# Kernel optimization log

Measured on AMD Instinct MI355X. Metric: run time of the kernel, lower is better.

The kernel has to match this reference:

```python
import jax, jax.numpy as jnp
import numpy as np

N, E, H = 50000, 800000, 4
DIM_IN, DIM_H, DIM_OUT, EDGE_DIM = 128, 64, 64, 16
NEG_ATT, NEG_OUT, BN_EPS = 0.2, 0.1, 1e-5


def batch_norm(x, gamma, beta):
    # training-mode BatchNorm1d over the node dimension
    mu = x.mean(0)
    var = x.var(0)
    return (x - mu) * jax.lax.rsqrt(var + BN_EPS) * gamma + beta


def gat_conv(x, src, dst, eattr, W, We, a_src, a_dst, a_edge, b, C):
    # x: [N, Fin] -> per-head projections h: [N, H, C]
    h = (x @ W).reshape(N, H, C)
    e = (eattr @ We).reshape(-1, H, C)               # [E2, H, C]
    al_src = (h * a_src).sum(-1)                     # [N, H]
    al_dst = (h * a_dst).sum(-1)                     # [N, H]
    al_edge = (e * a_edge).sum(-1)                   # [E2, H]
    logits = jax.nn.leaky_relu(al_src[src] + al_dst[dst] + al_edge, NEG_ATT)
    # segment softmax over destination-node neighborhoods
    m = jax.ops.segment_max(logits, dst, num_segments=N)
    ex = jnp.exp(logits - m[dst])
    denom = jax.ops.segment_sum(ex, dst, num_segments=N)
    alpha = ex / denom[dst]                          # [E2, H]
    msg = h[src] * alpha[:, :, None]                 # [E2, H, C]
    out = jax.ops.segment_sum(msg, dst, num_segments=N)
    return out.reshape(N, H * C) + b


def setup_inputs():
    key = jax.random.key(0)
    ks = jax.random.split(key, 16)
    g = lambda k, sh, sc: jax.random.normal(k, sh, jnp.float32) * sc
    HID = H * DIM_H
    return {
        'x': g(ks[0], (N, DIM_IN), 1.0),
        'edge_index': jax.random.randint(ks[1], (2, E), 0, N),
        'edge_attr': g(ks[2], (E, EDGE_DIM), 1.0),
        'bn1_gamma': jnp.ones(DIM_IN, jnp.float32),
        'bn1_beta': jnp.zeros(DIM_IN, jnp.float32),
        'W1': g(ks[3], (DIM_IN, H * DIM_H), 0.06),
        'We1': g(ks[4], (EDGE_DIM, H * DIM_H), 0.06),
        'asrc1': g(ks[5], (1, H, DIM_H), 0.1),
        'adst1': g(ks[6], (1, H, DIM_H), 0.1),
        'aedge1': g(ks[7], (1, H, DIM_H), 0.1),
        'b1': jnp.zeros(H * DIM_H, jnp.float32),
        'bn2_gamma': jnp.ones(HID, jnp.float32),
        'bn2_beta': jnp.zeros(HID, jnp.float32),
        'W2': g(ks[8], (HID, H * DIM_OUT), 0.06),
        'We2': g(ks[9], (EDGE_DIM, H * DIM_OUT), 0.06),
        'asrc2': g(ks[10], (1, H, DIM_OUT), 0.1),
        'adst2': g(ks[11], (1, H, DIM_OUT), 0.1),
        'aedge2': g(ks[12], (1, H, DIM_OUT), 0.1),
        'b2': jnp.zeros(H * DIM_OUT, jnp.float32),
    }


def reference(x, edge_index, edge_attr, bn1_gamma, bn1_beta, W1, We1, asrc1, adst1, aedge1, b1,
              bn2_gamma, bn2_beta, W2, We2, asrc2, adst2, aedge2, b2):
    # PyG GATConv default add_self_loops=True with edge_attr fill_value='mean'
    loop = jnp.arange(N)
    src = jnp.concatenate([edge_index[0], loop])
    dst = jnp.concatenate([edge_index[1], loop])
    e_mean = edge_attr.mean(0)
    eattr = jnp.concatenate([edge_attr, jnp.broadcast_to(e_mean[None], (N, EDGE_DIM))], 0)

    lrelu = lambda v: jax.nn.leaky_relu(v, NEG_OUT)
    h = lrelu(batch_norm(x, bn1_gamma, bn1_beta))                 # dropout = identity (eval)
    h = lrelu(gat_conv(h, src, dst, eattr, W1, We1, asrc1, adst1, aedge1, b1, DIM_H))
    h = lrelu(batch_norm(h, bn2_gamma, bn2_beta))
    h = gat_conv(h, src, dst, eattr, W2, We2, asrc2, adst2, aedge2, b2, DIM_OUT)
    return lrelu(h), edge_index
```

## Files before the change

kernel.cpp:

```cpp
#include <hip/hip_runtime.h>
#include <hip/hip_bf16.h>

constexpr int N_  = 50000;
constexpr int E_  = 800000;
constexpr int E2_ = 850000;
constexpr int FIN = 128;
constexpr int FH  = 256;
constexpr float BN_EPS = 1e-5f;
constexpr float NEG_ATT = 0.2f;
constexpr float NEG_OUT = 0.1f;
constexpr size_t OUT0 = (size_t)N_ * FH;
constexpr size_t OUT1 = (size_t)2 * E_;
constexpr int SCAN_NBLK = (N_ + 255) / 256;
constexpr int ATTR_NBLK = 1024;

static inline int cdiv(int a, int b){ return (a + b - 1) / b; }

using short8 = __attribute__((ext_vector_type(8))) short;
using f32x4  = __attribute__((ext_vector_type(4))) float;
using f32x2  = __attribute__((ext_vector_type(2))) float;

#if __has_builtin(__builtin_amdgcn_cvt_pk_f32_fp8) && __has_builtin(__builtin_amdgcn_cvt_pk_fp8_f32)
#define FP8_HW 1
#else
#define FP8_HW 0
#endif

__device__ inline float lrelu(float v, float ns){ return v > 0.f ? v : ns * v; }

__device__ inline unsigned short bf16rne(float f){
    unsigned u = __float_as_uint(f);
    u += 0x7fffu + ((u >> 16) & 1u);
    return (unsigned short)(u >> 16);
}
__device__ inline float bf16lo(unsigned u){ return __uint_as_float(u << 16); }
__device__ inline float bf16hi(unsigned u){ return __uint_as_float(u & 0xffff0000u); }
__device__ inline float bf16f(unsigned short v){ return __uint_as_float((unsigned)v << 16); }

__device__ inline float fp8dec1(unsigned b){
    unsigned s = b >> 7;
    unsigned e = (b >> 3) & 15;
    unsigned m = b & 7;
    float v;
    if (e == 0) v = (float)m * 0.001953125f;
    else        v = __uint_as_float(((e + 120u) << 23) | (m << 20));
    return s ? -v : v;
}
__device__ inline unsigned fp8enc1(float f){
    unsigned u = __float_as_uint(f);
    unsigned s = (u >> 31) << 7;
    float af = fabsf(f);
    if (af >= 448.f) return s | 0x7Eu;
    if (af < 0.0009765625f) return s;
    if (af < 0.015625f){
        int q = (int)(af * 512.f + 0.5f);
        return s | (unsigned)q;
    }
    unsigned a = u & 0x7fffffffu;
    a += 0x7FFFFu + ((a >> 20) & 1u);
    int e8 = (int)(a >> 23) - 120;
    unsigned m8 = (a >> 20) & 7u;
    if (e8 > 15 || (e8 == 15 && m8 == 7u)) return s | 0x7Eu;
    return s | ((unsigned)e8 << 3) | m8;
}
__device__ inline void dec4(unsigned g, float& f0, float& f1, float& f2, float& f3){
#if FP8_HW
    f32x2 lo = __builtin_amdgcn_cvt_pk_f32_fp8((int)g, false);
    f32x2 hi = __builtin_amdgcn_cvt_pk_f32_fp8((int)g, true);
    f0 = lo[0]; f1 = lo[1]; f2 = hi[0]; f3 = hi[1];
#else
    f0 = fp8dec1(g & 255u); f1 = fp8dec1((g >> 8) & 255u);
    f2 = fp8dec1((g >> 16) & 255u); f3 = fp8dec1(g >> 24);
#endif
}

__global__ void k_sentinel(float* out, float v){ out[0] = v; }

__global__ void k_zero32(unsigned* p, int n){
    int i = blockIdx.x * blockDim.x + threadIdx.x;
    if (i < n) p[i] = 0u;
}

__global__ void k_w2t(const float* __restrict__ W, unsigned short* __restrict__ WT, int K){
    int i = blockIdx.x * blockDim.x + threadIdx.x;
    if (i >= K * 256) return;
    int k = i >> 8, c = i & 255;
    WT[(size_t)c * K + k] = bf16rne(W[i]);
}

__global__ void k_h2fp8(const unsigned short* __restrict__ hb, unsigned* __restrict__ h8){
    size_t tot = (size_t)N_ * 256 / 4;
    size_t step = (size_t)gridDim.x * blockDim.x;
    for (size_t i = blockIdx.x * (size_t)blockDim.x + threadIdx.x; i < tot; i += step){
        uint2 g = *reinterpret_cast<const uint2*>(hb + i * 4);
        float f0 = bf16lo(g.x), f1 = bf16hi(g.x), f2 = bf16lo(g.y), f3 = bf16hi(g.y);
#if FP8_HW
        int lo = __builtin_amdgcn_cvt_pk_fp8_f32(f0, f1, 0, false);
        int pk = __builtin_amdgcn_cvt_pk_fp8_f32(f2, f3, lo, true);
        h8[i] = (unsigned)pk;
#else
        h8[i] = fp8enc1(f0) | (fp8enc1(f1) << 8) | (fp8enc1(f2) << 16) | (fp8enc1(f3) << 24);
#endif
    }
}

__global__ void k_bn_stats(const float* __restrict__ x, int F,
                           float* __restrict__ sum, float* __restrict__ sumsq){
    int gid = blockIdx.x * blockDim.x + threadIdx.x;
    int T = gridDim.x * blockDim.x;
    int c = gid % F;
    int r0 = gid / F;
    int rstep = T / F;
    float s = 0.f, s2 = 0.f;
    for (int r = r0; r < N_; r += rstep){
        float v = x[(size_t)r * F + c];
        s += v; s2 += v * v;
    }
    atomicAdd(&sum[c], s);
    atomicAdd(&sumsq[c], s2);
}

__global__ void k_bn_stats_b16(const unsigned short* __restrict__ x, int F,
                               float* __restrict__ sum, float* __restrict__ sumsq){
    int gid = blockIdx.x * blockDim.x + threadIdx.x;
    int T = gridDim.x * blockDim.x;
    int c = gid % F;
    int r0 = gid / F;
    int rstep = T / F;
    float s = 0.f, s2 = 0.f;
    for (int r = r0; r < N_; r += rstep){
        float v = bf16f(x[(size_t)r * F + c]);
        s += v; s2 += v * v;
    }
    atomicAdd(&sum[c], s);
    atomicAdd(&sumsq[c], s2);
}

__global__ void k_bn_apply_bf(const float* __restrict__ x, const float* __restrict__ sum,
                              const float* __restrict__ sumsq, const float* __restrict__ gamma,
                              const float* __restrict__ beta, unsigned short* __restrict__ out, int F){
    size_t tot = (size_t)N_ * F;
    size_t step = (size_t)gridDim.x * blockDim.x;
    for (size_t i = blockIdx.x * (size_t)blockDim.x + threadIdx.x; i < tot; i += step){
        int c = (int)(i % F);
        float mean = sum[c] / (float)N_;
        float var = sumsq[c] / (float)N_ - mean * mean;
        float v = (x[i] - mean) * rsqrtf(var + BN_EPS) * gamma[c] + beta[c];
        out[i] = bf16rne(lrelu(v, NEG_OUT));
    }
}

__global__ void k_bn_apply_b16(const unsigned short* __restrict__ x, const float* __restrict__ sum,
                               const float* __restrict__ sumsq, const float* __restrict__ gamma,
                               const float* __restrict__ beta, unsigned short* __restrict__ out, int F){
    size_t tot = (size_t)N_ * F;
    size_t step = (size_t)gridDim.x * blockDim.x;
    for (size_t i = blockIdx.x * (size_t)blockDim.x + threadIdx.x; i < tot; i += step){
        int c = (int)(i % F);
        float mean = sum[c] / (float)N_;
        float var = sumsq[c] / (float)N_ - mean * mean;
        float v = (bf16f(x[i]) - mean) * rsqrtf(var + BN_EPS) * gamma[c] + beta[c];
        out[i] = bf16rne(lrelu(v, NEG_OUT));
    }
}

__global__ __launch_bounds__(256) void k_gemm_mfma(const unsigned short* __restrict__ A,
                                                   const unsigned short* __restrict__ WT,
                                                   unsigned short* __restrict__ C, int M, int K){
    __shared__ unsigned short Al[64][32];
    __shared__ unsigned short Bl[64][32];
    int tid = threadIdx.x;
    int w = tid >> 6;
    int l = tid & 63;
    int row0 = blockIdx.x * 64;
    int col0 = blockIdx.y * 64;
    f32x4 acc[4];
    #pragma unroll
    for (int m = 0; m < 4; ++m) acc[m] = (f32x4){0.f, 0.f, 0.f, 0.f};

    int srow = tid >> 2;
    int skq  = (tid & 3) * 8;

    for (int k0 = 0; k0 < K; k0 += 32){
        {
            short8 v = {0,0,0,0,0,0,0,0};
            if (row0 + srow < M)
                v = *reinterpret_cast<const short8*>(A + (size_t)(row0 + srow) * K + k0 + skq);
            *reinterpret_cast<short8*>(&Al[srow][skq]) = v;
        }
        {
            short8 v = *reinterpret_cast<const short8*>(WT + (size_t)(col0 + srow) * K + k0 + skq);
            *reinterpret_cast<short8*>(&Bl[srow][skq]) = v;
        }
        __syncthreads();
        short8 b = *reinterpret_cast<const short8*>(&Bl[w * 16 + (l & 15)][8 * (l >> 4)]);
        #pragma unroll
        for (int m = 0; m < 4; ++m){
            short8 a = *reinterpret_cast<const short8*>(&Al[m * 16 + (l & 15)][8 * (l >> 4)]);
            acc[m] = __builtin_amdgcn_mfma_f32_16x16x32_bf16(a, b, acc[m], 0, 0, 0);
        }
        __syncthreads();
    }
    int ccol = col0 + w * 16 + (l & 15);
    #pragma unroll
    for (int m = 0; m < 4; ++m){
        #pragma unroll
        for (int r = 0; r < 4; ++r){
            int row = row0 + m * 16 + (l >> 4) * 4 + r;
            if (row < M) C[(size_t)row * 256 + ccol] = bf16rne(acc[m][r]);
        }
    }
}

__global__ __launch_bounds__(256) void k_al(const unsigned short* __restrict__ hb,
                                            const float* __restrict__ asrc,
                                            const float* __restrict__ adst,
                                            float* __restrict__ als, float* __restrict__ ald){
    int n = blockIdx.x * 4 + (threadIdx.x >> 6);
    if (n >= N_) return;
    int lane = threadIdx.x & 63;
    uint2 g = *reinterpret_cast<const uint2*>(hb + (size_t)n * 256 + lane * 4);
    float h0 = bf16lo(g.x), h1 = bf16hi(g.x), h2 = bf16lo(g.y), h3 = bf16hi(g.y);
    float4 as = *reinterpret_cast<const float4*>(asrc + lane * 4);
    float4 ad = *reinterpret_cast<const float4*>(adst + lane * 4);
    float ps = h0*as.x + h1*as.y + h2*as.z + h3*as.w;
    float pd = h0*ad.x + h1*ad.y + h2*ad.z + h3*ad.w;
    #pragma unroll
    for (int m = 1; m < 16; m <<= 1){
        ps += __shfl_xor(ps, m, 64);
        pd += __shfl_xor(pd, m, 64);
    }
    if ((lane & 15) == 0){
        int hd = lane >> 4;
        als[(size_t)n*4 + hd] = ps;
        ald[(size_t)n*4 + hd] = pd;
    }
}

__global__ __launch_bounds__(256) void k_attr_sum(const float* __restrict__ ea,
                                                  float* __restrict__ part){
    __shared__ float4 sdata[256];
    int tid = threadIdx.x;
    const float4* p = reinterpret_cast<const float4*>(ea);
    size_t step = (size_t)gridDim.x * 256;
    size_t end = (size_t)E_ * 4;
    size_t j = (size_t)blockIdx.x * 256 + tid;
    float4 a0 = make_float4(0.f,0.f,0.f,0.f), a1 = a0, a2 = a0, a3 = a0;
    for (; j + 3 * step < end; j += 4 * step){
        float4 v0 = p[j], v1 = p[j + step], v2 = p[j + 2*step], v3 = p[j + 3*step];
        a0.x += v0.x; a0.y += v0.y; a0.z += v0.z; a0.w += v0.w;
        a1.x += v1.x; a1.y += v1.y; a1.z += v1.z; a1.w += v1.w;
        a2.x += v2.x; a2.y += v2.y; a2.z += v2.z; a2.w += v2.w;
        a3.x += v3.x; a3.y += v3.y; a3.z += v3.z; a3.w += v3.w;
    }
    for (; j < end; j += step){
        float4 v = p[j];
        a0.x += v.x; a0.y += v.y; a0.z += v.z; a0.w += v.w;
    }
    a0.x += a1.x + a2.x + a3.x;  a0.y += a1.y + a2.y + a3.y;
    a0.z += a1.z + a2.z + a3.z;  a0.w += a1.w + a2.w + a3.w;
    sdata[tid] = a0;
    __syncthreads();
    #pragma unroll
    for (int s = 128; s >= 4; s >>= 1){
        if (tid < s){
            float4 o = sdata[tid + s];
            float4 m = sdata[tid];
            m.x += o.x; m.y += o.y; m.z += o.z; m.w += o.w;
            sdata[tid] = m;
        }
        __syncthreads();
    }
    if (tid < 4){
        float4 m = sdata[tid];
        float* pp = part + (size_t)blockIdx.x * 16 + tid * 4;
        pp[0] = m.x; pp[1] = m.y; pp[2] = m.z; pp[3] = m.w;
    }
}

__global__ __launch_bounds__(256) void k_attr_fin(const float* __restrict__ part,
                                                  float* __restrict__ asum){
    __shared__ float sd[256];
    int t = threadIdx.x;
    int col = t & 15, seg = t >> 4;
    float s = 0.f;
    for (int b = seg; b < ATTR_NBLK; b += 16) s += part[(size_t)b * 16 + col];
    sd[t] = s;
    __syncthreads();
    #pragma unroll
    for (int off = 128; off >= 16; off >>= 1){
        if (t < off) sd[t] += sd[t + off];
        __syncthreads();
    }
    if (t < 16) asum[t] = sd[t];
}

__global__ void k_prep(const float* __restrict__ We, const float* __restrict__ aedge,
                       const float* __restrict__ asum, float* __restrict__ V,
                       float* __restrict__ alloop){
    __shared__ float Vs[64];
    int t = threadIdx.x;
    int k = t >> 2, hd = t & 3;
    float s = 0.f;
    for (int c = 0; c < 64; ++c) s += We[k * 256 + hd * 64 + c] * aedge[hd * 64 + c];
    Vs[t] = s;
    V[t] = s;
    __syncthreads();
    if (t < 4){
        float r = 0.f;
        for (int kk = 0; kk < 16; ++kk) r += (asum[kk] / (float)E_) * Vs[kk * 4 + t];
        alloop[t] = r;
    }
}

__global__ void k_al_edge(const float* __restrict__ ea, const float* __restrict__ V,
                          float* __restrict__ ale){
    int idx = blockIdx.x * blockDim.x + threadIdx.x;
    if (idx >= E_ * 4) return;
    int e = idx >> 2, hd = idx & 3;
    const float* ep = ea + (size_t)e * 16;
    float s = 0.f;
    #pragma unroll
    for (int k = 0; k < 16; ++k) s += ep[k] * V[k * 4 + hd];
    ale[idx] = s;
}

__global__ void k_count(const int* __restrict__ ei, int* __restrict__ counts){
    int e = blockIdx.x * blockDim.x + threadIdx.x;
    if (e >= E2_) return;
    int d = (e < E_) ? ei[E_ + e] : (e - E_);
    atomicAdd(&counts[d], 1);
}

__global__ __launch_bounds__(256) void k_scan_local(const int* __restrict__ counts,
                                                    int* __restrict__ rs,
                                                    int* __restrict__ bsum){
    __shared__ int sd[256];
    int t = threadIdx.x;
    int idx = blockIdx.x * 256 + t;
    int c = (idx < N_) ? counts[idx] : 0;
    sd[t] = c;
    __syncthreads();
    #pragma unroll
    for (int off = 1; off < 256; off <<= 1){
        int o = (t >= off) ? sd[t - off] : 0;
        __syncthreads();
        sd[t] += o;
        __syncthreads();
    }
    if (idx < N_) rs[idx] = sd[t] - c;
    if (t == 255) bsum[blockIdx.x] = sd[255];
}

__global__ __launch_bounds__(256) void k_scan_block(const int* __restrict__ bsum,
                                                    int* __restrict__ boff,
                                                    int* __restrict__ rs){
    __shared__ int sd[256];
    int t = threadIdx.x;
    int v = (t < SCAN_NBLK) ? bsum[t] : 0;
    sd[t] = v;
    __syncthreads();
    #pragma unroll
    for (int off = 1; off < 256; off <<= 1){
        int o = (t >= off) ? sd[t - off] : 0;
        __syncthreads();
        sd[t] += o;
        __syncthreads();
    }
    if (t < SCAN_NBLK) boff[t] = sd[t] - v;
    if (t == 0) rs[N_] = E2_;
}

__global__ __launch_bounds__(256) void k_scan_add(int* __restrict__ rs,
                                                  const int* __restrict__ boff){
    int idx = blockIdx.x * 256 + threadIdx.x;
    if (idx < N_) rs[idx] += boff[blockIdx.x];
}

__global__ void k_scatter(const int* __restrict__ ei, const int* __restrict__ rs,
                          int* __restrict__ cursor, int2* __restrict__ sedge){
    int e = blockIdx.x * blockDim.x + threadIdx.x;
    if (e >= E2_) return;
    int s, d;
    if (e < E_){ s = ei[e]; d = ei[E_ + e]; }
    else { s = e - E_; d = s; }
    int slot = rs[d] + atomicAdd(&cursor[d], 1);
    sedge[slot] = make_int2(s, e);
}

#define MERGE4(OFF) { \
    float mo  = __shfl_xor(m,   OFF, 64); \
    float dno = __shfl_xor(den, OFF, 64); \
    float o0=__shfl_xor(a0,OFF,64), o1=__shfl_xor(a1,OFF,64), o2=__shfl_xor(a2,OFF,64), o3=__shfl_xor(a3,OFF,64); \
    float o4=__shfl_xor(a4,OFF,64), o5=__shfl_xor(a5,OFF,64), o6=__shfl_xor(a6,OFF,64), o7=__shfl_xor(a7,OFF,64); \
    float o8=__shfl_xor(a8,OFF,64), o9=__shfl_xor(a9,OFF,64), oA=__shfl_xor(aA,OFF,64), oB=__shfl_xor(aB,OFF,64); \
    float oC=__shfl_xor(aC,OFF,64), oD=__shfl_xor(aD,OFF,64), oE=__shfl_xor(aE,OFF,64), oF=__shfl_xor(aF,OFF,64); \
    float M = fmaxf(m, mo); \
    float sS = __expf(m - M), sO = __expf(mo - M); \
    den = den*sS + dno*sO; \
    a0=a0*sS+o0*sO; a1=a1*sS+o1*sO; a2=a2*sS+o2*sO; a3=a3*sS+o3*sO; \
    a4=a4*sS+o4*sO; a5=a5*sS+o5*sO; a6=a6*sS+o6*sO; a7=a7*sS+o7*sO; \
    a8=a8*sS+o8*sO; a9=a9*sS+o9*sO; aA=aA*sS+oA*sO; aB=aB*sS+oB*sO; \
    aC=aC*sS+oC*sO; aD=aD*sS+oD*sO; aE=aE*sS+oE*sO; aF=aF*sS+oF*sO; \
    m = M; }

template<bool BF16OUT>
__global__ __launch_bounds__(256) void k_aggregate4(const unsigned char* __restrict__ hb8,
        const float* __restrict__ als, const float* __restrict__ ald,
        const float* __restrict__ ale, const float* __restrict__ alloop,
        const int* __restrict__ rs, const int2* __restrict__ sedge,
        const float* __restrict__ bias, void* __restrict__ outp){
    int n = blockIdx.x * 4 + (threadIdx.x >> 6);
    if (n >= N_) return;
    int lane = threadIdx.x & 63;
    int q  = lane >> 4;
    int sl = lane & 15;
    int col0 = sl * 16;
    int hd = sl >> 2;
    float aldn = ald[(size_t)n * 4 + hd];
    float alp  = alloop[hd];
    int i0 = rs[n], i1 = rs[n + 1];
    float m = -3.0e38f, den = 0.f;
    float a0=0.f,a1=0.f,a2=0.f,a3=0.f,a4=0.f,a5=0.f,a6=0.f,a7=0.f;
    float a8=0.f,a9=0.f,aA=0.f,aB=0.f,aC=0.f,aD=0.f,aE=0.f,aF=0.f;
    for (int i = i0 + q; i < i1; i += 4){
        int2 se = sedge[i];
        int s   = se.x;
        int eid = se.y;
        float alE = (eid < E_) ? ale[(size_t)eid * 4 + hd] : alp;
        float lg = als[(size_t)s * 4 + hd] + aldn + alE;
        lg = lrelu(lg, NEG_ATT);
        float mn = fmaxf(m, lg);
        float sc = __expf(m - mn);
        float p  = __expf(lg - mn);
        den = den * sc + p;
        uint4 g = *reinterpret_cast<const uint4*>(hb8 + (size_t)s * 256 + col0);
        float t0, t1, t2, t3;
        dec4(g.x, t0, t1, t2, t3);
        a0 = a0*sc + p*t0;  a1 = a1*sc + p*t1;  a2 = a2*sc + p*t2;  a3 = a3*sc + p*t3;
        dec4(g.y, t0, t1, t2, t3);
        a4 = a4*sc + p*t0;  a5 = a5*sc + p*t1;  a6 = a6*sc + p*t2;  a7 = a7*sc + p*t3;
        dec4(g.z, t0, t1, t2, t3);
        a8 = a8*sc + p*t0;  a9 = a9*sc + p*t1;  aA = aA*sc + p*t2;  aB = aB*sc + p*t3;
        dec4(g.w, t0, t1, t2, t3);
        aC = aC*sc + p*t0;  aD = aD*sc + p*t1;  aE = aE*sc + p*t2;  aF = aF*sc + p*t3;
        m = mn;
    }
    MERGE4(16)
    MERGE4(32)
    float inv = 1.f / den;
    float v0, v1, v2, v3;
    if      (q == 0){ v0 = a0; v1 = a1; v2 = a2; v3 = a3; }
    else if (q == 1){ v0 = a4; v1 = a5; v2 = a6; v3 = a7; }
    else if (q == 2){ v0 = a8; v1 = a9; v2 = aA; v3 = aB; }
    else            { v0 = aC; v1 = aD; v2 = aE; v3 = aF; }
    int wc = col0 + q * 4;
    float4 b4 = *reinterpret_cast<const float4*>(bias + wc);
    float r0 = lrelu(v0 * inv + b4.x, NEG_OUT);
    float r1 = lrelu(v1 * inv + b4.y, NEG_OUT);
    float r2 = lrelu(v2 * inv + b4.z, NEG_OUT);
    float r3 = lrelu(v3 * inv + b4.w, NEG_OUT);
    if (BF16OUT){
        ushort4 pk;
        pk.x = bf16rne(r0); pk.y = bf16rne(r1); pk.z = bf16rne(r2); pk.w = bf16rne(r3);
        *reinterpret_cast<ushort4*>((unsigned short*)outp + (size_t)n * 256 + wc) = pk;
    } else {
        *reinterpret_cast<float4*>((float*)outp + (size_t)n * 256 + wc) =
            make_float4(r0, r1, r2, r3);
    }
}

__global__ void k_edge_store(const int* __restrict__ ei, float* __restrict__ out){
    int j = blockIdx.x * blockDim.x + threadIdx.x;
    if (j >= (int)OUT1) return;
    out[j] = (float)ei[j];
}

extern "C" void kernel_launch(void* const* d_in, const int* in_sizes, int n_in,
                              void* d_out, int out_size, void* d_ws, size_t ws_size,
                              hipStream_t stream){
    const float* x    = (const float*)d_in[0];
    const int*   ei   = (const int*)d_in[1];
    const float* ea   = (const float*)d_in[2];
    const float* bn1g = (const float*)d_in[3];
    const float* bn1b = (const float*)d_in[4];
    const float* W1   = (const float*)d_in[5];
    const float* We1  = (const float*)d_in[6];
    const float* as1  = (const float*)d_in[7];
    const float* ad1  = (const float*)d_in[8];
    const float* ae1  = (const float*)d_in[9];
    const float* b1   = (const float*)d_in[10];
    const float* bn2g = (const float*)d_in[11];
    const float* bn2b = (const float*)d_in[12];
    const float* W2   = (const float*)d_in[13];
    const float* We2  = (const float*)d_in[14];
    const float* as2  = (const float*)d_in[15];
    const float* ad2  = (const float*)d_in[16];
    const float* ae2  = (const float*)d_in[17];
    const float* b2   = (const float*)d_in[18];
    float* out = (float*)d_out;

    bool ok = (n_in >= 19)
           && (in_sizes[0] == N_ * FIN)
           && (in_sizes[1] == 2 * E_)
           && (in_sizes[2] == E_ * 16)
           && (out_size == (int)(OUT0 + OUT1));
    if (!ok){ k_sentinel<<<1,1,0,stream>>>(out, 7777.f); return; }

    char* w = (char*)d_ws;
    size_t off = 0;
    auto alloc = [&](size_t bytes) -> void* {
        off = (off + 255) & ~(size_t)255;
        void* p = w + off;
        off += bytes;
        return p;
    };
    float* stats  = (float*)alloc(512 * 4);
    float* asum   = (float*)alloc(16 * 4);
    float* apart  = (float*)alloc((size_t)ATTR_NBLK * 16 * 4);
    float* Vbuf   = (float*)alloc(64 * 4);
    float* alloop = (float*)alloc(4 * 4);
    float* als    = (float*)alloc((size_t)N_ * 4 * 4);
    float* ald    = (float*)alloc((size_t)N_ * 4 * 4);
    float* ale    = (float*)alloc((size_t)E_ * 4 * 4);
    int*   rs     = (int*)alloc((size_t)(N_ + 1) * 4);
    int*   counts = (int*)alloc((size_t)N_ * 4);
    int*   cursor = (int*)alloc((size_t)N_ * 4);
    int*   bsum   = (int*)alloc((size_t)SCAN_NBLK * 4);
    int*   boff   = (int*)alloc((size_t)SCAN_NBLK * 4);
    int2*  sedge  = (int2*)alloc((size_t)E2_ * 8);
    unsigned short* WT1 = (unsigned short*)alloc((size_t)256 * FIN * 2);
    unsigned short* WT2 = (unsigned short*)alloc((size_t)256 * FH * 2);
    unsigned short* bufC = (unsigned short*)alloc((size_t)N_ * 256 * 2);
    unsigned short* hbuf = (unsigned short*)alloc((size_t)N_ * 256 * 2);
    unsigned char*  hbuf8 = (unsigned char*)alloc((size_t)N_ * 256);
    unsigned short* bufB = (unsigned short*)alloc((size_t)N_ * 256 * 2);
    if (off > ws_size){ k_sentinel<<<1,1,0,stream>>>(out, 5555.f); return; }

    float* ssum = stats;
    float* ssq  = stats + 256;
    const int GX = cdiv(N_, 64);

    k_zero32<<<cdiv(N_,256),256,0,stream>>>((unsigned*)counts, N_);
    k_zero32<<<cdiv(N_,256),256,0,stream>>>((unsigned*)cursor, N_);
    k_count<<<cdiv(E2_,256),256,0,stream>>>(ei, counts);
    k_scan_local<<<SCAN_NBLK,256,0,stream>>>(counts, rs, bsum);
    k_scan_block<<<1,256,0,stream>>>(bsum, boff, rs);
    k_scan_add<<<SCAN_NBLK,256,0,stream>>>(rs, boff);
    k_scatter<<<cdiv(E2_,256),256,0,stream>>>(ei, rs, cursor, sedge);

    k_zero32<<<2,256,0,stream>>>((unsigned*)stats, 512);
    k_attr_sum<<<ATTR_NBLK,256,0,stream>>>(ea, apart);
    k_attr_fin<<<1,256,0,stream>>>(apart, asum);
    k_w2t<<<FIN,256,0,stream>>>(W1, WT1, FIN);
    k_w2t<<<FH,256,0,stream>>>(W2, WT2, FH);

    k_bn_stats<<<256,256,0,stream>>>(x, FIN, ssum, ssq);
    k_bn_apply_bf<<<2048,256,0,stream>>>(x, ssum, ssq, bn1g, bn1b, bufC, FIN);

    k_gemm_mfma<<<dim3(GX,4),256,0,stream>>>(bufC, WT1, hbuf, N_, FIN);
    k_h2fp8<<<2048,256,0,stream>>>(hbuf, (unsigned*)hbuf8);
    k_al<<<cdiv(N_,4),256,0,stream>>>(hbuf, as1, ad1, als, ald);
    k_prep<<<1,64,0,stream>>>(We1, ae1, asum, Vbuf, alloop);
    k_al_edge<<<cdiv(E_*4,256),256,0,stream>>>(ea, Vbuf, ale);
    k_aggregate4<true><<<cdiv(N_,4),256,0,stream>>>(hbuf8, als, ald, ale, alloop,
                                                    rs, sedge, b1, bufB);

    k_zero32<<<2,256,0,stream>>>((unsigned*)stats, 512);
    k_bn_stats_b16<<<256,256,0,stream>>>(bufB, FH, ssum, ssq);
    k_bn_apply_b16<<<2048,256,0,stream>>>(bufB, ssum, ssq, bn2g, bn2b, bufC, FH);

    k_gemm_mfma<<<dim3(GX,4),256,0,stream>>>(bufC, WT2, hbuf, N_, FH);
    k_h2fp8<<<2048,256,0,stream>>>(hbuf, (unsigned*)hbuf8);
    k_al<<<cdiv(N_,4),256,0,stream>>>(hbuf, as2, ad2, als, ald);
    k_prep<<<1,64,0,stream>>>(We2, ae2, asum, Vbuf, alloop);
    k_al_edge<<<cdiv(E_*4,256),256,0,stream>>>(ea, Vbuf, ale);
    k_aggregate4<false><<<cdiv(N_,4),256,0,stream>>>(hbuf8, als, ald, ale, alloop,
                                                     rs, sedge, b2, out);

    k_edge_store<<<cdiv((int)OUT1,256),256,0,stream>>>(ei, out + OUT0);
}
```

Baseline: 473.7 us.

## Split segment softmax into max/denominator pass and fuse fp8 conversion into GEMM epilogue

A new k_smax kernel computes the per-node, per-head softmax max and inverse denominator in one thread per (node, head). The aggregation kernel then accumulates exp(lg - max) * h without online rescaling and merges lanes with a plain sum instead of the max/rescale merge. The GEMM epilogue also writes an fp8 copy of its output directly, removing the separate bf16-to-fp8 conversion pass. In exchange there is an extra kernel launch and a second pass over the edge lists and attention logits, and the GEMM epilogue does narrow byte stores.

Measured after the change: 525.6 us. +11.0%, slower.

```diff
diff --git a/kernel.cpp b/kernel.cpp
--- a/kernel.cpp
+++ b/kernel.cpp
@@ -73,6 +73,13 @@
     f2 = fp8dec1((g >> 16) & 255u); f3 = fp8dec1(g >> 24);
 #endif
 }
+__device__ inline unsigned char fp8b(float f){
+#if FP8_HW
+    return (unsigned char)(__builtin_amdgcn_cvt_pk_fp8_f32(f, f, 0, false) & 0xff);
+#else
+    return (unsigned char)fp8enc1(f);
+#endif
+}
 
 __global__ void k_sentinel(float* out, float v){ out[0] = v; }
 
@@ -86,22 +93,6 @@
     if (i >= K * 256) return;
     int k = i >> 8, c = i & 255;
     WT[(size_t)c * K + k] = bf16rne(W[i]);
-}
-
-__global__ void k_h2fp8(const unsigned short* __restrict__ hb, unsigned* __restrict__ h8){
-    size_t tot = (size_t)N_ * 256 / 4;
-    size_t step = (size_t)gridDim.x * blockDim.x;
-    for (size_t i = blockIdx.x * (size_t)blockDim.x + threadIdx.x; i < tot; i += step){
-        uint2 g = *reinterpret_cast<const uint2*>(hb + i * 4);
-        float f0 = bf16lo(g.x), f1 = bf16hi(g.x), f2 = bf16lo(g.y), f3 = bf16hi(g.y);
-#if FP8_HW
-        int lo = __builtin_amdgcn_cvt_pk_fp8_f32(f0, f1, 0, false);
-        int pk = __builtin_amdgcn_cvt_pk_fp8_f32(f2, f3, lo, true);
-        h8[i] = (unsigned)pk;
-#else
-        h8[i] = fp8enc1(f0) | (fp8enc1(f1) << 8) | (fp8enc1(f2) << 16) | (fp8enc1(f3) << 24);
-#endif
-    }
 }
 
 __global__ void k_bn_stats(const float* __restrict__ x, int F,
@@ -166,7 +157,8 @@
 
 __global__ __launch_bounds__(256) void k_gemm_mfma(const unsigned short* __restrict__ A,
                                                    const unsigned short* __restrict__ WT,
-                                                   unsigned short* __restrict__ C, int M, int K){
+                                                   unsigned short* __restrict__ C,
+                                                   unsigned char* __restrict__ C8, int M, int K){
     __shared__ unsigned short Al[64][32];
     __shared__ unsigned short Bl[64][32];
     int tid = threadIdx.x;
@@ -207,7 +199,11 @@
         #pragma unroll
         for (int r = 0; r < 4; ++r){
             int row = row0 + m * 16 + (l >> 4) * 4 + r;
-            if (row < M) C[(size_t)row * 256 + ccol] = bf16rne(acc[m][r]);
+            if (row < M){
+                float f = acc[m][r];
+                C[(size_t)row * 256 + ccol]  = bf16rne(f);
+                C8[(size_t)row * 256 + ccol] = fp8b(f);
+            }
         }
     }
 }
@@ -388,26 +384,39 @@
     sedge[slot] = make_int2(s, e);
 }
 
-#define MERGE4(OFF) { \
-    float mo  = __shfl_xor(m,   OFF, 64); \
-    float dno = __shfl_xor(den, OFF, 64); \
-    float o0=__shfl_xor(a0,OFF,64), o1=__shfl_xor(a1,OFF,64), o2=__shfl_xor(a2,OFF,64), o3=__shfl_xor(a3,OFF,64); \
-    float o4=__shfl_xor(a4,OFF,64), o5=__shfl_xor(a5,OFF,64), o6=__shfl_xor(a6,OFF,64), o7=__shfl_xor(a7,OFF,64); \
-    float o8=__shfl_xor(a8,OFF,64), o9=__shfl_xor(a9,OFF,64), oA=__shfl_xor(aA,OFF,64), oB=__shfl_xor(aB,OFF,64); \
-    float oC=__shfl_xor(aC,OFF,64), oD=__shfl_xor(aD,OFF,64), oE=__shfl_xor(aE,OFF,64), oF=__shfl_xor(aF,OFF,64); \
-    float M = fmaxf(m, mo); \
-    float sS = __expf(m - M), sO = __expf(mo - M); \
-    den = den*sS + dno*sO; \
-    a0=a0*sS+o0*sO; a1=a1*sS+o1*sO; a2=a2*sS+o2*sO; a3=a3*sS+o3*sO; \
-    a4=a4*sS+o4*sO; a5=a5*sS+o5*sO; a6=a6*sS+o6*sO; a7=a7*sS+o7*sO; \
-    a8=a8*sS+o8*sO; a9=a9*sS+o9*sO; aA=aA*sS+oA*sO; aB=aB*sS+oB*sO; \
-    aC=aC*sS+oC*sO; aD=aD*sS+oD*sO; aE=aE*sS+oE*sO; aF=aF*sS+oF*sO; \
-    m = M; }
+__global__ __launch_bounds__(256) void k_smax(const int* __restrict__ rs,
+        const int2* __restrict__ sedge, const float* __restrict__ als,
+        const float* __restrict__ ald, const float* __restrict__ ale,
+        const float* __restrict__ alloop, float2* __restrict__ mxden){
+    int idx = blockIdx.x * 256 + threadIdx.x;
+    if (idx >= N_ * 4) return;
+    int n = idx >> 2, hd = idx & 3;
+    float aldn = ald[idx];
+    float alp  = alloop[hd];
+    int i0 = rs[n], i1 = rs[n + 1];
+    float m = -3.0e38f, den = 0.f;
+    for (int i = i0; i < i1; ++i){
+        int2 se = sedge[i];
+        float alE = (se.y < E_) ? ale[(size_t)se.y * 4 + hd] : alp;
+        float lg = lrelu(als[(size_t)se.x * 4 + hd] + aldn + alE, NEG_ATT);
+        float mn = fmaxf(m, lg);
+        den = den * __expf(m - mn) + __expf(lg - mn);
+        m = mn;
+    }
+    mxden[idx] = make_float2(m, 1.f / den);
+}
+
+#define SUMM(OFF) { \
+    a0+=__shfl_xor(a0,OFF,64); a1+=__shfl_xor(a1,OFF,64); a2+=__shfl_xor(a2,OFF,64); a3+=__shfl_xor(a3,OFF,64); \
+    a4+=__shfl_xor(a4,OFF,64); a5+=__shfl_xor(a5,OFF,64); a6+=__shfl_xor(a6,OFF,64); a7+=__shfl_xor(a7,OFF,64); \
+    a8+=__shfl_xor(a8,OFF,64); a9+=__shfl_xor(a9,OFF,64); aA+=__shfl_xor(aA,OFF,64); aB+=__shfl_xor(aB,OFF,64); \
+    aC+=__shfl_xor(aC,OFF,64); aD+=__shfl_xor(aD,OFF,64); aE+=__shfl_xor(aE,OFF,64); aF+=__shfl_xor(aF,OFF,64); }
 
 template<bool BF16OUT>
 __global__ __launch_bounds__(256) void k_aggregate4(const unsigned char* __restrict__ hb8,
         const float* __restrict__ als, const float* __restrict__ ald,
         const float* __restrict__ ale, const float* __restrict__ alloop,
+        const float2* __restrict__ mxden,
         const int* __restrict__ rs, const int2* __restrict__ sedge,
         const float* __restrict__ bias, void* __restrict__ outp){
     int n = blockIdx.x * 4 + (threadIdx.x >> 6);
@@ -419,36 +428,30 @@
     int hd = sl >> 2;
     float aldn = ald[(size_t)n * 4 + hd];
     float alp  = alloop[hd];
+    float2 md  = mxden[(size_t)n * 4 + hd];
+    float mxn = md.x, invden = md.y;
     int i0 = rs[n], i1 = rs[n + 1];
-    float m = -3.0e38f, den = 0.f;
     float a0=0.f,a1=0.f,a2=0.f,a3=0.f,a4=0.f,a5=0.f,a6=0.f,a7=0.f;
     float a8=0.f,a9=0.f,aA=0.f,aB=0.f,aC=0.f,aD=0.f,aE=0.f,aF=0.f;
     for (int i = i0 + q; i < i1; i += 4){
         int2 se = sedge[i];
         int s   = se.x;
-        int eid = se.y;
-        float alE = (eid < E_) ? ale[(size_t)eid * 4 + hd] : alp;
-        float lg = als[(size_t)s * 4 + hd] + aldn + alE;
-        lg = lrelu(lg, NEG_ATT);
-        float mn = fmaxf(m, lg);
-        float sc = __expf(m - mn);
-        float p  = __expf(lg - mn);
-        den = den * sc + p;
+        float alE = (se.y < E_) ? ale[(size_t)se.y * 4 + hd] : alp;
+        float lg = lrelu(als[(size_t)s * 4 + hd] + aldn + alE, NEG_ATT);
+        float p  = __expf(lg - mxn);
         uint4 g = *reinterpret_cast<const uint4*>(hb8 + (size_t)s * 256 + col0);
         float t0, t1, t2, t3;
         dec4(g.x, t0, t1, t2, t3);
-        a0 = a0*sc + p*t0;  a1 = a1*sc + p*t1;  a2 = a2*sc + p*t2;  a3 = a3*sc + p*t3;
+        a0 += p*t0;  a1 += p*t1;  a2 += p*t2;  a3 += p*t3;
         dec4(g.y, t0, t1, t2, t3);
-        a4 = a4*sc + p*t0;  a5 = a5*sc + p*t1;  a6 = a6*sc + p*t2;  a7 = a7*sc + p*t3;
+        a4 += p*t0;  a5 += p*t1;  a6 += p*t2;  a7 += p*t3;
         dec4(g.z, t0, t1, t2, t3);
-        a8 = a8*sc + p*t0;  a9 = a9*sc + p*t1;  aA = aA*sc + p*t2;  aB = aB*sc + p*t3;
+        a8 += p*t0;  a9 += p*t1;  aA += p*t2;  aB += p*t3;
         dec4(g.w, t0, t1, t2, t3);
-        aC = aC*sc + p*t0;  aD = aD*sc + p*t1;  aE = aE*sc + p*t2;  aF = aF*sc + p*t3;
-        m = mn;
-    }
-    MERGE4(16)
-    MERGE4(32)
-    float inv = 1.f / den;
+        aC += p*t0;  aD += p*t1;  aE += p*t2;  aF += p*t3;
+    }
+    SUMM(16)
+    SUMM(32)
     float v0, v1, v2, v3;
     if      (q == 0){ v0 = a0; v1 = a1; v2 = a2; v3 = a3; }
     else if (q == 1){ v0 = a4; v1 = a5; v2 = a6; v3 = a7; }
@@ -456,10 +459,10 @@
     else            { v0 = aC; v1 = aD; v2 = aE; v3 = aF; }
     int wc = col0 + q * 4;
     float4 b4 = *reinterpret_cast<const float4*>(bias + wc);
-    float r0 = lrelu(v0 * inv + b4.x, NEG_OUT);
-    float r1 = lrelu(v1 * inv + b4.y, NEG_OUT);
-    float r2 = lrelu(v2 * inv + b4.z, NEG_OUT);
-    float r3 = lrelu(v3 * inv + b4.w, NEG_OUT);
+    float r0 = lrelu(v0 * invden + b4.x, NEG_OUT);
+    float r1 = lrelu(v1 * invden + b4.y, NEG_OUT);
+    float r2 = lrelu(v2 * invden + b4.z, NEG_OUT);
+    float r3 = lrelu(v3 * invden + b4.w, NEG_OUT);
     if (BF16OUT){
         ushort4 pk;
         pk.x = bf16rne(r0); pk.y = bf16rne(r1); pk.z = bf16rne(r2); pk.w = bf16rne(r3);
@@ -522,6 +525,7 @@
     float* alloop = (float*)alloc(4 * 4);
     float* als    = (float*)alloc((size_t)N_ * 4 * 4);
     float* ald    = (float*)alloc((size_t)N_ * 4 * 4);
+    float2* mxden = (float2*)alloc((size_t)N_ * 4 * 8);
     float* ale    = (float*)alloc((size_t)E_ * 4 * 4);
     int*   rs     = (int*)alloc((size_t)(N_ + 1) * 4);
     int*   counts = (int*)alloc((size_t)N_ * 4);
@@ -540,6 +544,7 @@
     float* ssum = stats;
     float* ssq  = stats + 256;
     const int GX = cdiv(N_, 64);
+    const int NB4 = cdiv(N_ * 4, 256);
 
     k_zero32<<<cdiv(N_,256),256,0,stream>>>((unsigned*)counts, N_);
     k_zero32<<<cdiv(N_,256),256,0,stream>>>((unsigned*)cursor, N_);
@@ -558,24 +563,24 @@
     k_bn_stats<<<256,256,0,stream>>>(x, FIN, ssum, ssq);
     k_bn_apply_bf<<<2048,256,0,stream>>>(x, ssum, ssq, bn1g, bn1b, bufC, FIN);
 
-    k_gemm_mfma<<<dim3(GX,4),256,0,stream>>>(bufC, WT1, hbuf, N_, FIN);
-    k_h2fp8<<<2048,256,0,stream>>>(hbuf, (unsigned*)hbuf8);
+    k_gemm_mfma<<<dim3(GX,4),256,0,stream>>>(bufC, WT1, hbuf, hbuf8, N_, FIN);
     k_al<<<cdiv(N_,4),256,0,stream>>>(hbuf, as1, ad1, als, ald);
     k_prep<<<1,64,0,stream>>>(We1, ae1, asum, Vbuf, alloop);
     k_al_edge<<<cdiv(E_*4,256),256,0,stream>>>(ea, Vbuf, ale);
-    k_aggregate4<true><<<cdiv(N_,4),256,0,stream>>>(hbuf8, als, ald, ale, alloop,
+    k_smax<<<NB4,256,0,stream>>>(rs, sedge, als, ald, ale, alloop, mxden);
+    k_aggregate4<true><<<cdiv(N_,4),256,0,stream>>>(hbuf8, als, ald, ale, alloop, mxden,
                                                     rs, sedge, b1, bufB);
 
     k_zero32<<<2,256,0,stream>>>((unsigned*)stats, 512);
     k_bn_stats_b16<<<256,256,0,stream>>>(bufB, FH, ssum, ssq);
     k_bn_apply_b16<<<2048,256,0,stream>>>(bufB, ssum, ssq, bn2g, bn2b, bufC, FH);
 
-    k_gemm_mfma<<<dim3(GX,4),256,0,stream>>>(bufC, WT2, hbuf, N_, FH);
-    k_h2fp8<<<2048,256,0,stream>>>(hbuf, (unsigned*)hbuf8);
+    k_gemm_mfma<<<dim3(GX,4),256,0,stream>>>(bufC, WT2, hbuf, hbuf8, N_, FH);
     k_al<<<cdiv(N_,4),256,0,stream>>>(hbuf, as2, ad2, als, ald);
     k_prep<<<1,64,0,stream>>>(We2, ae2, asum, Vbuf, alloop);
     k_al_edge<<<cdiv(E_*4,256),256,0,stream>>>(ea, Vbuf, ale);
-    k_aggregate4<false><<<cdiv(N_,4),256,0,stream>>>(hbuf8, als, ald, ale, alloop,
+    k_smax<<<NB4,256,0,stream>>>(rs, sedge, als, ald, ale, alloop, mxden);
+    k_aggregate4<false><<<cdiv(N_,4),256,0,stream>>>(hbuf8, als, ald, ale, alloop, mxden,
                                                      rs, sedge, b2, out);
 
     k_edge_store<<<cdiv((int)OUT1,256),256,0,stream>>>(ei, out + OUT0);
```
